# Kernel optimization log

Hardware: AMD Instinct MI355X
Metric: run time of the kernel (lower is better)

Reference implementation:

```python
import jax, jax.numpy as jnp
import numpy as np

EMBED_DIM = 1024
NUM_HEADS = 16
HEAD_DIM = EMBED_DIM // NUM_HEADS


def setup_inputs() -> dict:
    key = jax.random.key(0)
    ks = jax.random.split(key, 11)
    B, S, D = 2, 2048, EMBED_DIM
    s = 1.0 / np.sqrt(D)
    inp = {
        "q": jax.random.normal(ks[0], (B, S, D), jnp.float32),
        "k": jax.random.normal(ks[1], (B, S, D), jnp.float32),
        "v": jax.random.normal(ks[2], (B, S, D), jnp.float32),
        # Linear params stored as (in, out) so y = x @ W + b
        "wq": jax.random.uniform(ks[3], (D, D), jnp.float32, -s, s),
        "bq": jax.random.uniform(ks[4], (D,), jnp.float32, -s, s),
        "wk": jax.random.uniform(ks[5], (D, D), jnp.float32, -s, s),
        "bk": jax.random.uniform(ks[6], (D,), jnp.float32, -s, s),
        "wv": jax.random.uniform(ks[7], (D, D), jnp.float32, -s, s),
        "bv": jax.random.uniform(ks[8], (D,), jnp.float32, -s, s),
        "wo": jax.random.uniform(ks[9], (D, D), jnp.float32, -s, s),
        "bo": jax.random.uniform(ks[10], (D,), jnp.float32, -s, s),
    }
    return inp


def reference(q, k, v, wq, bq, wk, bk, wv, bv, wo, bo):
    B, S, D = q.shape
    H, Hd = NUM_HEADS, HEAD_DIM
    temperature = Hd ** 0.5

    def proj(x, w, b):
        # (B, S, D) -> (B, H, S, Hd)
        y = x @ w + b
        return y.reshape(B, S, H, Hd).transpose(0, 2, 1, 3)

    qh = proj(q, wq, bq)
    kh = proj(k, wk, bk)
    vh = proj(v, wv, bv)

    # naive attention with materialized [B, H, S, S] scores (faithful to source)
    scores = jnp.einsum("bhqd,bhkd->bhqk", qh / temperature, kh)
    attn = jax.nn.softmax(scores, axis=-1)
    ctx = jnp.einsum("bhqk,bhkd->bhqd", attn, vh)

    ctx = ctx.transpose(0, 2, 1, 3).reshape(B, S, D)
    out = ctx @ wo + bo
    return out, attn
```

## Files before the change

### kernel.cpp

```cpp
#include <hip/hip_runtime.h>

#define S_   2048
#define D_   1024

typedef __attribute__((ext_vector_type(8))) __bf16 bf16x8;
typedef __attribute__((ext_vector_type(4))) __bf16 bf16x4;
typedef __attribute__((ext_vector_type(4))) float f32x4;
typedef __attribute__((ext_vector_type(4))) float float4v;
typedef __attribute__((ext_vector_type(2))) unsigned int u32x2;
typedef __attribute__((ext_vector_type(4))) unsigned int u32x4;

#define XQ_OFF   0
#define XK_OFF   4194304
#define XV_OFF   8388608
#define WQT_OFF  12582912
#define WKT_OFF  13631488
#define WVT_OFF  14680064
#define WOT_OFF  15728640
#define QH_OFF   16777216
#define KH_OFF   20971520
#define VHT_OFF  25165824
#define CTX_OFF  29360128
#define WS_BYTES 67108864ULL

#if __has_builtin(__builtin_amdgcn_exp2f)
#define EXP2(x) __builtin_amdgcn_exp2f(x)
#else
#define EXP2(x) __expf((x) * 0.69314718056f)
#endif
#define QSCALE 0.1803368801f

__device__ __forceinline__ unsigned short f2b(float f) {
  unsigned u = __builtin_bit_cast(unsigned, f);
  u += 0x7fffu + ((u >> 16) & 1u);
  return (unsigned short)(u >> 16);
}
__device__ __forceinline__ float b2f(unsigned s) {
  return __builtin_bit_cast(float, s << 16);
}

__global__ __launch_bounds__(256) void cvt_all(const float* __restrict__ q,
    const float* __restrict__ k, const float* __restrict__ v,
    const float* __restrict__ wq, const float* __restrict__ wk,
    const float* __restrict__ wv, const float* __restrict__ wo,
    short* __restrict__ ws) {
  __shared__ float tile[32][33];
  int b = blockIdx.x, tid = threadIdx.x;
  if (b < 12288) {
    int y = b >> 12, x = b & 4095;
    const float* src = (y == 0) ? q : (y == 1) ? k : v;
    short* dst = ws + (size_t)y * 4194304;
    size_t t = (size_t)x * 256 + tid;
    float4v f = *(const float4v*)(src + t * 4);
    u32x2 p;
    p[0] = (unsigned)f2b(f[0]) | ((unsigned)f2b(f[1]) << 16);
    p[1] = (unsigned)f2b(f[2]) | ((unsigned)f2b(f[3]) << 16);
    *(u32x2*)(dst + t * 4) = p;
    return;
  }
  int b2 = b - 12288;
  int z = b2 >> 10, rem = b2 & 1023;
  int by = rem >> 5, bx = rem & 31;
  const float* W = (z == 0) ? wq : (z == 1) ? wk : (z == 2) ? wv : wo;
  short* Wt = ws + WQT_OFF + (size_t)z * 1048576;
  int tx = tid & 31, ty = tid >> 5;
#pragma unroll
  for (int i = 0; i < 4; ++i)
    tile[ty + i * 8][tx] =
        W[(size_t)(by * 32 + ty + i * 8) * D_ + bx * 32 + tx];
  __syncthreads();
#pragma unroll
  for (int i = 0; i < 4; ++i)
    Wt[(size_t)(bx * 32 + ty + i * 8) * D_ + by * 32 + tx] =
        (short)f2b(tile[tx][ty + i * 8]);
}

__device__ __forceinline__ void stage_tile(const short* __restrict__ g,
                                           short* l, int w, int lane) {
  int lrow = lane >> 3, lcol = (lane & 7) * 8;
#pragma unroll
  for (int c = 0; c < 4; ++c) {
    int seg = c * 4 + w;
    const short* gp = g + (size_t)(seg * 8 + lrow) * 1024 + lcol;
    short* lp = l + seg * 512 + lane * 8;
    __builtin_amdgcn_global_load_lds(
        (const __attribute__((address_space(1))) void*)gp,
        (__attribute__((address_space(3))) void*)lp, 16, 0, 0);
  }
}

__global__ __launch_bounds__(256) void gemm_bf16(short* __restrict__ ws,
    const float* __restrict__ bq, const float* __restrict__ bk,
    const float* __restrict__ bv, const float* __restrict__ bo,
    float* __restrict__ out, int mode_base) {
  const int tid = threadIdx.x, lane = tid & 63, w = tid >> 6;
  const int wm = w >> 1, wn = w & 1;
  const int ln15 = lane & 15, g = lane >> 4;
  const int bm = blockIdx.y, bn = blockIdx.x;
  const int mode = (mode_base == 3) ? 3 : (int)blockIdx.z;

  const short* A; const short* Bt; const float* bias;
  if (mode == 0)      { A = ws + XQ_OFF;  Bt = ws + WQT_OFF; bias = bq; }
  else if (mode == 1) { A = ws + XK_OFF;  Bt = ws + WKT_OFF; bias = bk; }
  else if (mode == 2) { A = ws + XV_OFF;  Bt = ws + WVT_OFF; bias = bv; }
  else                { A = ws + CTX_OFF; Bt = ws + WOT_OFF; bias = bo; }

  __shared__ short smem[2][2][8192];
  short (*sA)[8192] = smem[0];
  short (*sB)[8192] = smem[1];

  f32x4 acc[4][4] = {};

  const short* Ab = A + (size_t)bm * 128 * 1024;
  const short* Bb = Bt + (size_t)bn * 128 * 1024;

  stage_tile(Ab, sA[0], w, lane);
  stage_tile(Bb, sB[0], w, lane);
  __syncthreads();

  int cur = 0;
#pragma unroll 1
  for (int kt = 0; kt < 16; ++kt) {
    if (kt < 15) {
      stage_tile(Ab + (kt + 1) * 64, sA[cur ^ 1], w, lane);
      stage_tile(Bb + (kt + 1) * 64, sB[cur ^ 1], w, lane);
    }
#pragma unroll
    for (int kk = 0; kk < 2; ++kk) {
      bf16x8 af[4], bfr[4];
#pragma unroll
      for (int m = 0; m < 4; ++m)
        af[m] = *(const bf16x8*)&sA[cur][(wm * 64 + m * 16 + ln15) * 64 + kk * 32 + g * 8];
#pragma unroll
      for (int n = 0; n < 4; ++n)
        bfr[n] = *(const bf16x8*)&sB[cur][(wn * 64 + n * 16 + ln15) * 64 + kk * 32 + g * 8];
#pragma unroll
      for (int m = 0; m < 4; ++m)
#pragma unroll
        for (int n = 0; n < 4; ++n)
          acc[m][n] = __builtin_amdgcn_mfma_f32_16x16x32_bf16(af[m], bfr[n], acc[m][n], 0, 0, 0);
    }
    __syncthreads();
    cur ^= 1;
  }

  float bb[4];
#pragma unroll
  for (int n = 0; n < 4; ++n) bb[n] = bias[bn * 128 + wn * 64 + n * 16 + ln15];

  if (mode == 3) {
#pragma unroll
    for (int m = 0; m < 4; ++m) {
      int row0 = bm * 128 + wm * 64 + m * 16 + g * 4;
#pragma unroll
      for (int n = 0; n < 4; ++n) {
        int col = bn * 128 + wn * 64 + n * 16 + ln15;
#pragma unroll
        for (int r = 0; r < 4; ++r)
          out[(size_t)(row0 + r) * 1024 + col] = acc[m][n][r] + bb[n];
      }
    }
    return;
  }

  float sc = (mode == 0) ? QSCALE : 1.0f;
  short (*tile)[136] = (short(*)[136])smem;
#pragma unroll
  for (int m = 0; m < 4; ++m)
#pragma unroll
    for (int n = 0; n < 4; ++n)
#pragma unroll
      for (int r = 0; r < 4; ++r)
        tile[wm * 64 + m * 16 + g * 4 + r][wn * 64 + n * 16 + ln15] =
            (short)f2b((acc[m][n][r] + bb[n]) * sc);
  __syncthreads();

  const int bq_ = bm >> 4;
  const int sml = bm & 15;
  if (mode == 0) {
    int h_out = tid >> 7, rt = (tid >> 4) & 7, h = (tid >> 3) & 1, sub = tid & 7;
    int bh = bq_ * 16 + bn * 2 + h_out;
    size_t base = QH_OFF + (((size_t)bh * 128 + sml * 8 + rt) * 2 + h) * 512;
#pragma unroll
    for (int i = 0; i < 8; ++i) {
      int l = sub * 8 + i;
      u32x4 v = *(const u32x4*)&tile[rt * 16 + (l & 15)]
                                    [h_out * 64 + h * 32 + (l >> 4) * 8];
      *(u32x4*)&ws[base + l * 8] = v;
    }
  } else if (mode == 1) {
    int kt_l = tid >> 7, h_out = (tid >> 6) & 1, f = (tid >> 3) & 7, sub = tid & 7;
    int bh = bq_ * 16 + bn * 2 + h_out;
    size_t base = KH_OFF + (((size_t)bh * 32 + sml * 2 + kt_l) * 8 + f) * 512;
#pragma unroll
    for (int i = 0; i < 8; ++i) {
      int l = sub * 8 + i;
      u32x4 v = *(const u32x4*)&tile[kt_l * 64 + (f >> 1) * 16 + (l & 15)]
                                    [h_out * 64 + (f & 1) * 32 + (l >> 4) * 8];
      *(u32x4*)&ws[base + l * 8] = v;
    }
  } else {
    int kt_l = tid >> 7, h_out = (tid >> 6) & 1, fv = (tid >> 3) & 7, sub = tid & 7;
    int bh = bq_ * 16 + bn * 2 + h_out;
    size_t base = VHT_OFF + (((size_t)bh * 32 + sml * 2 + kt_l) * 8 + fv) * 512;
#pragma unroll
    for (int i = 0; i < 8; ++i) {
      int l = sub * 8 + i;
      int hd = h_out * 64 + (fv >> 1) * 16 + (l & 15);
      int s0 = kt_l * 64 + (fv & 1) * 32 + (l >> 4) * 8;
      u32x4 pk;
#pragma unroll
      for (int e2 = 0; e2 < 4; ++e2) {
        unsigned lo = (unsigned short)tile[s0 + e2 * 2][hd];
        unsigned hi = (unsigned short)tile[s0 + e2 * 2 + 1][hd];
        pk[e2] = lo | (hi << 16);
      }
      *(u32x4*)&ws[base + l * 8] = pk;
    }
  }
}

__global__ __launch_bounds__(512) void attn_k(short* __restrict__ ws,
                                              float* __restrict__ attn) {
  const int tid = threadIdx.x, lane = tid & 63, w = tid >> 6;
  const int ln15 = lane & 15, g = lane >> 4;
  int bid = blockIdx.x;
  int qt = (bid >> 3) & 15;
  int bh = (bid & 7) + 8 * (bid >> 7);
  const int q0 = qt * 128;

  const short* qhF = ws + QH_OFF + (((size_t)bh * 128 + qt * 8 + w) * 2) * 512;
  const short* khF = ws + KH_OFF + (size_t)bh * 131072;
  const short* vhF = ws + VHT_OFF + (size_t)bh * 131072;

  __shared__ short Pbig[128][264];

  bf16x8 qf0 = *(const bf16x8*)&qhF[lane * 8];
  bf16x8 qf1 = *(const bf16x8*)&qhF[512 + lane * 8];

  float ps0 = 0.f, ps1 = 0.f;
#pragma unroll 1
  for (int kt = 0; kt < 32; ++kt) {
    const short* kb = khF + kt * 4096 + lane * 8;
    bf16x8 ka[8];
#pragma unroll
    for (int f = 0; f < 8; ++f) ka[f] = *(const bf16x8*)&kb[f * 512];
#pragma unroll
    for (int m = 0; m < 4; ++m) {
      f32x4 c = {0.f, 0.f, 0.f, 0.f};
      c = __builtin_amdgcn_mfma_f32_16x16x32_bf16(ka[m * 2], qf0, c, 0, 0, 0);
      c = __builtin_amdgcn_mfma_f32_16x16x32_bf16(ka[m * 2 + 1], qf1, c, 0, 0, 0);
      ps0 += EXP2(c[0]) + EXP2(c[1]);
      ps1 += EXP2(c[2]) + EXP2(c[3]);
    }
  }
  float ps = ps0 + ps1;
  ps += __shfl_xor(ps, 16, 64);
  ps += __shfl_xor(ps, 32, 64);
  float ri = 1.0f / ps;

  f32x4 cacc[4] = {};
#pragma unroll 1
  for (int s = 0; s < 8; ++s) {
#pragma unroll
    for (int j = 0; j < 4; ++j) {
      const int kt = s * 4 + j;
      const short* kb = khF + kt * 4096 + lane * 8;
#pragma unroll
      for (int m = 0; m < 4; ++m) {
        bf16x8 ka0 = *(const bf16x8*)&kb[(m * 2) * 512];
        bf16x8 ka1 = *(const bf16x8*)&kb[(m * 2 + 1) * 512];
        f32x4 c = {0.f, 0.f, 0.f, 0.f};
        c = __builtin_amdgcn_mfma_f32_16x16x32_bf16(ka0, qf0, c, 0, 0, 0);
        c = __builtin_amdgcn_mfma_f32_16x16x32_bf16(ka1, qf1, c, 0, 0, 0);
        bf16x4 pb;
        pb[0] = (__bf16)(EXP2(c[0]) * ri);
        pb[1] = (__bf16)(EXP2(c[1]) * ri);
        pb[2] = (__bf16)(EXP2(c[2]) * ri);
        pb[3] = (__bf16)(EXP2(c[3]) * ri);
        *(bf16x4*)&Pbig[w * 16 + ln15][j * 64 + m * 16 + g * 4] = pb;
      }
      const short* vb_ = vhF + kt * 4096 + lane * 8;
      bf16x8 vb[8];
#pragma unroll
      for (int f = 0; f < 8; ++f) vb[f] = *(const bf16x8*)&vb_[f * 512];
#pragma unroll
      for (int kk = 0; kk < 2; ++kk) {
        bf16x8 pa =
            *(const bf16x8*)&Pbig[w * 16 + ln15][j * 64 + kk * 32 + g * 8];
#pragma unroll
        for (int n = 0; n < 4; ++n)
          cacc[n] = __builtin_amdgcn_mfma_f32_16x16x32_bf16(
              pa, vb[n * 2 + kk], cacc[n], 0, 0, 0);
      }
    }

    float* ab = attn + ((size_t)(bh * 2048 + q0 + w * 16)) * 2048 + s * 256 +
                lane * 4;
#pragma unroll
    for (int r = 0; r < 16; ++r) {
      u32x2 pv = *(const u32x2*)&Pbig[w * 16 + r][lane * 4];
      float4v o;
      o[0] = b2f(pv[0] & 0xffffu);
      o[1] = b2f(pv[0] >> 16);
      o[2] = b2f(pv[1] & 0xffffu);
      o[3] = b2f(pv[1] >> 16);
      *(float4v*)(ab + (size_t)r * 2048) = o;
    }
  }

  {
    short* Pw = &Pbig[w * 16][0];
#pragma unroll
    for (int n = 0; n < 4; ++n)
#pragma unroll
      for (int r = 0; r < 4; ++r)
        Pw[(g * 4 + r) * 264 + n * 16 + ln15] = (short)f2b(cacc[n][r]);
    int b = bh >> 4, h = bh & 15;
    int row = lane >> 3, col = (lane & 7) * 8;
#pragma unroll
    for (int i = 0; i < 2; ++i) {
      int q = q0 + w * 16 + i * 8 + row;
      u32x4 pk = *(const u32x4*)&Pw[(i * 8 + row) * 264 + col];
      *(u32x4*)&ws[CTX_OFF + ((size_t)(b * 2048 + q)) * 1024 + h * 64 + col] = pk;
    }
  }
}

extern "C" void kernel_launch(void* const* d_in, const int* in_sizes, int n_in,
                              void* d_out, int out_size, void* d_ws, size_t ws_size,
                              hipStream_t stream) {
  const float* q  = (const float*)d_in[0];
  const float* k  = (const float*)d_in[1];
  const float* v  = (const float*)d_in[2];
  const float* wq = (const float*)d_in[3];
  const float* bq = (const float*)d_in[4];
  const float* wk = (const float*)d_in[5];
  const float* bk = (const float*)d_in[6];
  const float* wv = (const float*)d_in[7];
  const float* bv = (const float*)d_in[8];
  const float* wo = (const float*)d_in[9];
  const float* bo = (const float*)d_in[10];
  float* out  = (float*)d_out;
  float* attn = out + 4194304;
  short* ws = (short*)d_ws;
  if (ws_size < WS_BYTES) return;

  cvt_all<<<dim3(16384), 256, 0, stream>>>(q, k, v, wq, wk, wv, wo, ws);
  gemm_bf16<<<dim3(8, 32, 3), 256, 0, stream>>>(ws, bq, bk, bv, bo, out, 0);
  attn_k<<<dim3(512), 512, 0, stream>>>(ws, attn);
  gemm_bf16<<<dim3(8, 32, 1), 256, 0, stream>>>(ws, bq, bk, bv, bo, out, 3);
}
```

Baseline: 302.8 us.

## Single-pass attention with key-split waves and deferred softmax normalization

The attention kernel no longer computes QK^T twice (once for the row sums, once for the probabilities). It now processes 16 query rows per step. The 8 waves split the 2048 keys, store unnormalized exp values in a full-row LDS buffer, and reduce the row sums through shared memory. PV is split across waves by output column group and key half, and the partial results are combined through LDS, with normalization applied on the attn store and the context store. This trades the redundant matmul and exp work for extra block barriers, a larger LDS footprint, and a cross-wave reduction on every 16-row group.

```diff
diff --git a/kernel.cpp b/kernel.cpp
--- a/kernel.cpp
+++ b/kernel.cpp
@@ -220,8 +220,8 @@
   }
 }
 
-__global__ __launch_bounds__(512) void attn_k(short* __restrict__ ws,
-                                              float* __restrict__ attn) {
+__global__ __launch_bounds__(512, 4) void attn_k(short* __restrict__ ws,
+                                                 float* __restrict__ attn) {
   const int tid = threadIdx.x, lane = tid & 63, w = tid >> 6;
   const int ln15 = lane & 15, g = lane >> 4;
   int bid = blockIdx.x;
@@ -229,42 +229,29 @@
   int bh = (bid & 7) + 8 * (bid >> 7);
   const int q0 = qt * 128;
 
-  const short* qhF = ws + QH_OFF + (((size_t)bh * 128 + qt * 8 + w) * 2) * 512;
+  const short* qhF = ws + QH_OFF + (size_t)bh * 131072;
   const short* khF = ws + KH_OFF + (size_t)bh * 131072;
   const short* vhF = ws + VHT_OFF + (size_t)bh * 131072;
 
-  __shared__ short Pbig[128][264];
-
-  bf16x8 qf0 = *(const bf16x8*)&qhF[lane * 8];
-  bf16x8 qf1 = *(const bf16x8*)&qhF[512 + lane * 8];
-
-  float ps0 = 0.f, ps1 = 0.f;
+  __shared__ short Prow[16][2050];
+  __shared__ float rs[8][16];
+  __shared__ float ritot[16];
+  __shared__ float4v pbuf[4][64];
+
+  const int n_pv = w & 3, kh16 = (w >> 2) * 16, w4 = w * 4;
+  const int b_ = bh >> 4, h_ = bh & 15;
+
 #pragma unroll 1
-  for (int kt = 0; kt < 32; ++kt) {
-    const short* kb = khF + kt * 4096 + lane * 8;
-    bf16x8 ka[8];
-#pragma unroll
-    for (int f = 0; f < 8; ++f) ka[f] = *(const bf16x8*)&kb[f * 512];
-#pragma unroll
-    for (int m = 0; m < 4; ++m) {
-      f32x4 c = {0.f, 0.f, 0.f, 0.f};
-      c = __builtin_amdgcn_mfma_f32_16x16x32_bf16(ka[m * 2], qf0, c, 0, 0, 0);
-      c = __builtin_amdgcn_mfma_f32_16x16x32_bf16(ka[m * 2 + 1], qf1, c, 0, 0, 0);
-      ps0 += EXP2(c[0]) + EXP2(c[1]);
-      ps1 += EXP2(c[2]) + EXP2(c[3]);
-    }
-  }
-  float ps = ps0 + ps1;
-  ps += __shfl_xor(ps, 16, 64);
-  ps += __shfl_xor(ps, 32, 64);
-  float ri = 1.0f / ps;
-
-  f32x4 cacc[4] = {};
-#pragma unroll 1
-  for (int s = 0; s < 8; ++s) {
+  for (int qg = 0; qg < 8; ++qg) {
+    const int rt = qt * 8 + qg;
+    const short* qb = qhF + (size_t)rt * 1024;
+    bf16x8 qf0 = *(const bf16x8*)&qb[lane * 8];
+    bf16x8 qf1 = *(const bf16x8*)&qb[512 + lane * 8];
+
+    float ps0 = 0.f, ps1 = 0.f;
 #pragma unroll
     for (int j = 0; j < 4; ++j) {
-      const int kt = s * 4 + j;
+      const int kt = w4 + j;
       const short* kb = khF + kt * 4096 + lane * 8;
 #pragma unroll
       for (int m = 0; m < 4; ++m) {
@@ -273,56 +260,72 @@
         f32x4 c = {0.f, 0.f, 0.f, 0.f};
         c = __builtin_amdgcn_mfma_f32_16x16x32_bf16(ka0, qf0, c, 0, 0, 0);
         c = __builtin_amdgcn_mfma_f32_16x16x32_bf16(ka1, qf1, c, 0, 0, 0);
+        float e0 = EXP2(c[0]), e1 = EXP2(c[1]);
+        float e2 = EXP2(c[2]), e3 = EXP2(c[3]);
+        ps0 += e0 + e1;
+        ps1 += e2 + e3;
         bf16x4 pb;
-        pb[0] = (__bf16)(EXP2(c[0]) * ri);
-        pb[1] = (__bf16)(EXP2(c[1]) * ri);
-        pb[2] = (__bf16)(EXP2(c[2]) * ri);
-        pb[3] = (__bf16)(EXP2(c[3]) * ri);
-        *(bf16x4*)&Pbig[w * 16 + ln15][j * 64 + m * 16 + g * 4] = pb;
-      }
+        pb[0] = (__bf16)e0; pb[1] = (__bf16)e1;
+        pb[2] = (__bf16)e2; pb[3] = (__bf16)e3;
+        *(bf16x4*)&Prow[ln15][kt * 64 + m * 16 + g * 4] = pb;
+      }
+    }
+    float ps = ps0 + ps1;
+    ps += __shfl_xor(ps, 16, 64);
+    ps += __shfl_xor(ps, 32, 64);
+    if (lane < 16) rs[w][lane] = ps;
+
+    asm volatile("s_waitcnt lgkmcnt(0)" ::: "memory");
+    __builtin_amdgcn_s_barrier();
+
+    f32x4 cacc = {0.f, 0.f, 0.f, 0.f};
+#pragma unroll
+    for (int t2 = 0; t2 < 16; ++t2) {
+      const int kt = kh16 + t2;
       const short* vb_ = vhF + kt * 4096 + lane * 8;
-      bf16x8 vb[8];
-#pragma unroll
-      for (int f = 0; f < 8; ++f) vb[f] = *(const bf16x8*)&vb_[f * 512];
 #pragma unroll
       for (int kk = 0; kk < 2; ++kk) {
-        bf16x8 pa =
-            *(const bf16x8*)&Pbig[w * 16 + ln15][j * 64 + kk * 32 + g * 8];
-#pragma unroll
-        for (int n = 0; n < 4; ++n)
-          cacc[n] = __builtin_amdgcn_mfma_f32_16x16x32_bf16(
-              pa, vb[n * 2 + kk], cacc[n], 0, 0, 0);
-      }
-    }
-
-    float* ab = attn + ((size_t)(bh * 2048 + q0 + w * 16)) * 2048 + s * 256 +
-                lane * 4;
-#pragma unroll
-    for (int r = 0; r < 16; ++r) {
-      u32x2 pv = *(const u32x2*)&Pbig[w * 16 + r][lane * 4];
-      float4v o;
-      o[0] = b2f(pv[0] & 0xffffu);
-      o[1] = b2f(pv[0] >> 16);
-      o[2] = b2f(pv[1] & 0xffffu);
-      o[3] = b2f(pv[1] >> 16);
-      *(float4v*)(ab + (size_t)r * 2048) = o;
-    }
-  }
-
-  {
-    short* Pw = &Pbig[w * 16][0];
-#pragma unroll
-    for (int n = 0; n < 4; ++n)
-#pragma unroll
-      for (int r = 0; r < 4; ++r)
-        Pw[(g * 4 + r) * 264 + n * 16 + ln15] = (short)f2b(cacc[n][r]);
-    int b = bh >> 4, h = bh & 15;
-    int row = lane >> 3, col = (lane & 7) * 8;
-#pragma unroll
-    for (int i = 0; i < 2; ++i) {
-      int q = q0 + w * 16 + i * 8 + row;
-      u32x4 pk = *(const u32x4*)&Pw[(i * 8 + row) * 264 + col];
-      *(u32x4*)&ws[CTX_OFF + ((size_t)(b * 2048 + q)) * 1024 + h * 64 + col] = pk;
+        bf16x8 pa = *(const bf16x8*)&Prow[ln15][kt * 64 + kk * 32 + g * 8];
+        bf16x8 vb = *(const bf16x8*)&vb_[(n_pv * 2 + kk) * 512];
+        cacc = __builtin_amdgcn_mfma_f32_16x16x32_bf16(pa, vb, cacc, 0, 0, 0);
+      }
+    }
+
+#pragma unroll
+    for (int rr = 0; rr < 2; ++rr) {
+      const int r = w * 2 + rr;
+      float s = 0.f;
+#pragma unroll
+      for (int ww = 0; ww < 8; ++ww) s += rs[ww][r];
+      const float ri = 1.0f / s;
+      if (lane == 0) ritot[r] = ri;
+      float* ab = attn +
+                  ((size_t)(bh * 2048 + q0 + qg * 16 + r)) * 2048 + lane * 4;
+#pragma unroll
+      for (int c = 0; c < 8; ++c) {
+        u32x2 pv = *(const u32x2*)&Prow[r][c * 256 + lane * 4];
+        float4v o;
+        o[0] = b2f(pv[0] & 0xffffu) * ri;
+        o[1] = b2f(pv[0] >> 16) * ri;
+        o[2] = b2f(pv[1] & 0xffffu) * ri;
+        o[3] = b2f(pv[1] >> 16) * ri;
+        *(float4v*)(ab + c * 256) = o;
+      }
+    }
+
+    if (w >= 4) pbuf[w - 4][lane] = cacc;
+    asm volatile("s_waitcnt lgkmcnt(0)" ::: "memory");
+    __builtin_amdgcn_s_barrier();
+
+    if (w < 4) {
+      float4v oth = pbuf[w][lane];
+#pragma unroll
+      for (int rr = 0; rr < 4; ++rr) {
+        int qrow = q0 + qg * 16 + g * 4 + rr;
+        float val = (cacc[rr] + oth[rr]) * ritot[g * 4 + rr];
+        ws[CTX_OFF + ((size_t)(b_ * 2048 + qrow)) * 1024 + h_ * 64 +
+           w * 16 + ln15] = (short)f2b(val);
+      }
     }
   }
 }
```

After: 295.5 us. 2.4% less time.
